# Kernel tuning notes

Hardware: AMD Instinct MI355X
Metric: run time of the kernel (lower is better)

## Reference

```python
import jax, jax.numpy as jnp
import numpy as np

SEQ = 2048
DIM = 4096
N_HEADS = 32
N_KV_HEADS = 8
HEAD_DIM = DIM // N_HEADS  # 128
ROPE_THETA = 500000.0


def setup_inputs() -> dict:
    key = jax.random.key(0)
    ks = jax.random.split(key, 5)
    s = 0.02  # keep activations numerically tame
    return {
        "x": jax.random.normal(ks[0], (SEQ, DIM), dtype=jnp.float32),
        "wq": jax.random.normal(ks[1], (DIM, DIM), dtype=jnp.float32) * s,
        "wk": jax.random.normal(ks[2], (N_KV_HEADS * HEAD_DIM, DIM), dtype=jnp.float32) * s,
        "wv": jax.random.normal(ks[3], (N_KV_HEADS * HEAD_DIM, DIM), dtype=jnp.float32) * s,
        "wo": jax.random.normal(ks[4], (DIM, DIM), dtype=jnp.float32) * s,
    }


def _rope(t):
    # t: [S, H, D]; pairs (t[...,2i], t[...,2i+1]) rotated by angle pos * theta^(-i/(D/2)),
    # matching torch.view_as_complex on x.view(S, -1, 2) * polar(1, pos*freq).
    S, H, D = t.shape
    half = D // 2
    freqs = 1.0 / (ROPE_THETA ** (jnp.arange(half, dtype=jnp.float32) / half))
    ang = jnp.arange(S, dtype=jnp.float32)[:, None] * freqs[None, :]  # [S, half]
    cos = jnp.cos(ang)[:, None, :]  # [S, 1, half]
    sin = jnp.sin(ang)[:, None, :]
    tr = t.reshape(S, H, half, 2)
    x0, x1 = tr[..., 0], tr[..., 1]
    r0 = x0 * cos - x1 * sin
    r1 = x0 * sin + x1 * cos
    return jnp.stack([r0, r1], axis=-1).reshape(S, H, D)


def reference(x, wq, wk, wv, wo):
    S = x.shape[0]
    group = N_HEADS // N_KV_HEADS
    # Per-head projections (batched over heads instead of python loop)
    q = jnp.einsum("sd,hkd->shk", x, wq.reshape(N_HEADS, HEAD_DIM, DIM))        # [S,H,D]
    k = jnp.einsum("sd,hkd->shk", x, wk.reshape(N_KV_HEADS, HEAD_DIM, DIM))     # [S,Hkv,D]
    v = jnp.einsum("sd,hkd->shk", x, wv.reshape(N_KV_HEADS, HEAD_DIM, DIM))     # [S,Hkv,D]
    q = _rope(q)
    k = _rope(k)
    # GQA: q head h uses kv head h // group -> repeat kv heads consecutively
    kf = jnp.repeat(k, group, axis=1)  # [S,H,D]
    vf = jnp.repeat(v, group, axis=1)  # [S,H,D]
    scores = jnp.einsum("shd,thd->hst", q, kf) / jnp.sqrt(jnp.float32(HEAD_DIM))
    causal = jnp.tril(jnp.ones((S, S), dtype=bool))
    scores = jnp.where(causal[None], scores, -jnp.inf)
    probs = jax.nn.softmax(scores, axis=-1)
    out = jnp.einsum("hst,thd->shd", probs, vf).reshape(S, N_HEADS * HEAD_DIM)
    return out @ wo.T
```

## Files before the change

### kernel.cpp

```cpp
#include <hip/hip_runtime.h>
#include <stdint.h>
#include <math.h>

#define SEQ   2048
#define DIM   4096
#define NHEAD 32
#define NKV   8
#define HD    128
#define KVDIM (NKV*HD)

typedef __bf16 bf16x8 __attribute__((ext_vector_type(8)));
typedef float  f32x4  __attribute__((ext_vector_type(4)));

__device__ __forceinline__ uint16_t f2bf(float f) {
  uint32_t u = __float_as_uint(f);
  uint32_t r = (u + 0x7FFFu + ((u >> 16) & 1u)) >> 16;
  return (uint16_t)r;
}
__device__ __forceinline__ bf16x8 ld_frag(const uint16_t* p) {
  return *(const bf16x8*)p;
}
__device__ __forceinline__ void async_cp16(const void* g, void* lds) {
  __builtin_amdgcn_global_load_lds(
      (const __attribute__((address_space(1))) void*)g,
      (__attribute__((address_space(3))) void*)lds, 16, 0, 0);
}

__global__ __launch_bounds__(256) void k_conv_all(
    const float* __restrict__ x, const float* __restrict__ wq,
    const float* __restrict__ wk, const float* __restrict__ wv,
    uint16_t* __restrict__ xb, uint16_t* __restrict__ wqkvb) {
  size_t i = (size_t)blockIdx.x * 256 + threadIdx.x;
  const float* s; uint16_t* d; size_t off;
  if (i < 2097152)      { s = x;  d = xb;                 off = i; }
  else if (i < 6291456) { s = wq; d = wqkvb;              off = i - 2097152; }
  else if (i < 7340032) { s = wk; d = wqkvb + 16777216u;  off = i - 6291456; }
  else                  { s = wv; d = wqkvb + 20971520u;  off = i - 7340032; }
  const float4 v = ((const float4*)s)[off];
  ushort4 o;
  o.x = f2bf(v.x); o.y = f2bf(v.y); o.z = f2bf(v.z); o.w = f2bf(v.w);
  ((ushort4*)d)[off] = o;
}

__global__ __launch_bounds__(256) void k_conv(const float* __restrict__ s,
                                              uint16_t* __restrict__ d, int n4) {
  int i = blockIdx.x * 256 + threadIdx.x;
  if (i >= n4) return;
  const float4 v = ((const float4*)s)[i];
  ushort4 o;
  o.x = f2bf(v.x); o.y = f2bf(v.y); o.z = f2bf(v.z); o.w = f2bf(v.w);
  ((ushort4*)d)[i] = o;
}

#define GEMM_PROLOGUE(A, B)                                                     \
  __shared__ __align__(16) uint16_t sA[128 * 32];                               \
  __shared__ __align__(16) uint16_t sB[128 * 32];                               \
  const int tid  = threadIdx.x;                                                 \
  const int lane = tid & 63;                                                    \
  const int wv   = tid >> 6;                                                    \
  const int quad = lane >> 4;                                                   \
  const int l16  = lane & 15;                                                   \
  const int wm   = (wv & 1) << 6;                                               \
  const int wn   = (wv >> 1) << 6;                                              \
  const int p0 = tid, p1 = tid + 256;                                           \
  const int r0 = p0 >> 2, c0 = (p0 & 3) ^ ((r0 >> 1) & 3);                      \
  const int r1 = p1 >> 2, c1 = (p1 & 3) ^ ((r1 >> 1) & 3);                      \
  const uint16_t* gA0 = A + (size_t)(m0 + r0) * DIM + c0 * 8;                   \
  const uint16_t* gA1 = A + (size_t)(m0 + r1) * DIM + c1 * 8;                   \
  const uint16_t* gB0 = B + (size_t)(n0 + r0) * DIM + c0 * 8;                   \
  const uint16_t* gB1 = B + (size_t)(n0 + r1) * DIM + c1 * 8;                   \
  uint16_t* lA0 = sA + p0 * 8;                                                  \
  uint16_t* lA1 = sA + p1 * 8;                                                  \
  uint16_t* lB0 = sB + p0 * 8;                                                  \
  uint16_t* lB1 = sB + p1 * 8;                                                  \
  f32x4 acc[4][4] = {};                                                         \
  int offA[4], offB[4];                                                         \
  _Pragma("unroll")                                                             \
  for (int t = 0; t < 4; t++) {                                                 \
    int ml_ = wm + t * 16 + l16;                                                \
    offA[t] = (ml_ * 4 + (quad ^ ((ml_ >> 1) & 3))) * 8;                        \
    int nl_ = wn + t * 16 + l16;                                                \
    offB[t] = (nl_ * 4 + (quad ^ ((nl_ >> 1) & 3))) * 8;                        \
  }                                                                             \
  for (int k0 = 0; k0 < DIM; k0 += 32) {                                        \
    async_cp16(gA0 + k0, lA0);                                                  \
    async_cp16(gA1 + k0, lA1);                                                  \
    async_cp16(gB0 + k0, lB0);                                                  \
    async_cp16(gB1 + k0, lB1);                                                  \
    __syncthreads();                                                            \
    bf16x8 af[4], bfv[4];                                                       \
    _Pragma("unroll")                                                           \
    for (int t = 0; t < 4; t++) {                                               \
      af[t]  = ld_frag(sA + offA[t]);                                           \
      bfv[t] = ld_frag(sB + offB[t]);                                           \
    }                                                                           \
    _Pragma("unroll")                                                           \
    for (int mt = 0; mt < 4; mt++)                                              \
      _Pragma("unroll")                                                         \
      for (int nt = 0; nt < 4; nt++)                                            \
        acc[mt][nt] = __builtin_amdgcn_mfma_f32_16x16x32_bf16(af[mt], bfv[nt],  \
                                                              acc[mt][nt], 0, 0, 0); \
    __syncthreads();                                                            \
  }

__global__ __launch_bounds__(256) void k_gemm_qkv(
    const uint16_t* __restrict__ xb, const uint16_t* __restrict__ wqkvb,
    uint16_t* __restrict__ Qb, uint16_t* __restrict__ Kb, uint16_t* __restrict__ Vb)
{
  const int bx = blockIdx.x;
  const int m0 = blockIdx.y * 128;
  const int n0 = bx * 128;
  GEMM_PROLOGUE(xb, wqkvb)

  const int region = (bx < 32) ? 0 : (bx < 40 ? 1 : 2);
  uint16_t* outp; int ldC, cbase;
  if (region == 0)      { outp = Qb; ldC = DIM;   cbase = n0; }
  else if (region == 1) { outp = Kb; ldC = KVDIM; cbase = n0 - 4096; }
  else                  { outp = Vb; ldC = KVDIM; cbase = n0 - 5120; }

  #pragma unroll
  for (int mt = 0; mt < 4; mt++)
    #pragma unroll
    for (int nt = 0; nt < 4; nt++) {
      const int col = cbase + wn + nt * 16 + l16;
      const int d = col & 127;
      const float freq = expf(-0.20503693f * (float)(d >> 1));
      const float sgn = (d & 1) ? 1.0f : -1.0f;
      #pragma unroll
      for (int r = 0; r < 4; r++) {
        const int row = m0 + wm + mt * 16 + quad * 4 + r;
        float v = acc[mt][nt][r];
        if (region < 2) {
          float p = __shfl_xor(v, 1, 64);
          float ang = (float)row * freq;
          float sn, cs;
          sincosf(ang, &sn, &cs);
          v = v * cs + p * sn * sgn;
        }
        outp[(size_t)row * ldC + col] = f2bf(v);
      }
    }
}

__global__ __launch_bounds__(256) void k_gemm_o(
    const uint16_t* __restrict__ ab, const uint16_t* __restrict__ wob,
    float* __restrict__ out)
{
  const int m0 = blockIdx.y * 128;
  const int n0 = blockIdx.x * 128;
  GEMM_PROLOGUE(ab, wob)
  #pragma unroll
  for (int mt = 0; mt < 4; mt++)
    #pragma unroll
    for (int nt = 0; nt < 4; nt++)
      #pragma unroll
      for (int r = 0; r < 4; r++) {
        int row = m0 + wm + mt * 16 + quad * 4 + r;
        int col = n0 + wn + nt * 16 + l16;
        out[(size_t)row * DIM + col] = acc[mt][nt][r];
      }
}

__global__ __launch_bounds__(256) void k_vtrans(const uint16_t* __restrict__ Vb,
                                                uint16_t* __restrict__ VT) {
  __shared__ uint16_t t[64][72];
  const int s0 = blockIdx.x * 64;
  const int c0 = blockIdx.y * 64;
  const int tid = threadIdx.x;
  #pragma unroll
  for (int i = 0; i < 2; i++) {
    int idx = i * 256 + tid;
    int r = idx >> 3, ch = idx & 7;
    uint4 dv = *(const uint4*)(Vb + (size_t)(s0 + r) * KVDIM + c0 + ch * 8);
    *(uint4*)(&t[r][ch * 8]) = dv;
  }
  __syncthreads();
  const int kvh = c0 >> 7;
  const int dbase = c0 & 127;
  #pragma unroll
  for (int i = 0; i < 2; i++) {
    int idx = i * 256 + tid;
    int d = idx >> 3, sc = idx & 7;
    uint16_t tmp[8];
    #pragma unroll
    for (int j2 = 0; j2 < 8; j2++) tmp[j2] = t[sc * 8 + j2][d];
    *(uint4*)(VT + (size_t)kvh * HD * SEQ + (size_t)(dbase + d) * SEQ + s0 + sc * 8) = *(const uint4*)tmp;
  }
}

#define BKV 64
#define NPAIR 40
__device__ __constant__ uint8_t c_pair[NPAIR] = {
  12,16,20,24,28,29,32,33,36,37,40,41,44,45,46,48,49,50,52,53,54,56,57,58,60,61,62,63,
  8,25,42,59,
  4,21,38,55,
  0,17,34,51
};
__device__ __constant__ uint8_t c_base[16] = {0,1,2,3,4,6,8,10,12,15,18,21,24,28,32,36};

__global__ __launch_bounds__(256) void k_flash_split(
    const uint16_t* __restrict__ Qb, const uint16_t* __restrict__ Kb,
    const uint16_t* __restrict__ VT, uint16_t* __restrict__ Opart,
    float* __restrict__ ml)
{
  const int pair = c_pair[blockIdx.x];
  const int qt   = pair >> 2;
  const int seg  = pair & 3;
  const int h    = blockIdx.y;
  const int kvh  = h >> 2;
  const int slot = h * NPAIR + c_base[qt] + seg;
  const int tid  = threadIdx.x;
  const int lane = tid & 63;
  const int wv   = tid >> 6;
  const int quad = lane >> 4;
  const int l16  = lane & 15;
  const int q0   = qt * 128;

  __shared__ __align__(16) uint16_t sK[BKV * 128];
  __shared__ __align__(16) uint16_t sVT[HD * BKV];
  __shared__ __align__(16) uint16_t sP[4 * 32 * 72];

  const uint16_t* Kbase  = Kb + kvh * HD;
  const uint16_t* VTbase = VT + (size_t)kvh * HD * SEQ;

  bf16x8 qf[2][4];
  #pragma unroll
  for (int mt = 0; mt < 2; mt++)
    #pragma unroll
    for (int ks = 0; ks < 4; ks++)
      qf[mt][ks] = ld_frag(Qb + (size_t)(q0 + wv * 32 + mt * 16 + l16) * DIM + h * HD + ks * 32 + quad * 8);

  __align__(16) uint16_t ones_bits[8];
  #pragma unroll
  for (int j = 0; j < 8; j++) ones_bits[j] = (l16 == 0) ? 0x3F80 : 0;
  const bf16x8 onesf = *(const bf16x8*)ones_bits;

  f32x4 Oacc[2][8] = {};
  f32x4 Lacc[2] = {};

  const float scale = 0.08838834764831845f;
  const float MFIX = 12.0f;
  const int j0 = seg * 8;
  const int j1 = min(j0 + 8, 2 * (qt + 1));

  for (int j = j0; j < j1; j++) {
    const int t0 = j * BKV;
    #pragma unroll
    for (int i = 0; i < 4; i++) {
      int pos = i * 256 + tid;
      int row = pos >> 4, g = (pos & 15) ^ (row & 7);
      async_cp16(Kbase + (size_t)(t0 + row) * KVDIM + g * 8, sK + pos * 8);
      int vrow = pos >> 3, vg = (pos & 7) ^ (vrow & 7);
      async_cp16(VTbase + (size_t)vrow * SEQ + t0 + vg * 8, sVT + pos * 8);
    }
    __syncthreads();

    bool active = (t0 <= q0 + wv * 32 + 31);
    if (active) {
      f32x4 Sacc[2][4] = {};
      #pragma unroll
      for (int ks = 0; ks < 4; ks++) {
        bf16x8 kf[4];
        #pragma unroll
        for (int nt = 0; nt < 4; nt++)
          kf[nt] = ld_frag(sK + (nt * 16 + l16) * 128 + (((ks * 4 + quad) ^ (l16 & 7)) * 8));
        #pragma unroll
        for (int mt = 0; mt < 2; mt++)
          #pragma unroll
          for (int nt = 0; nt < 4; nt++)
            Sacc[mt][nt] = __builtin_amdgcn_mfma_f32_16x16x32_bf16(qf[mt][ks], kf[nt], Sacc[mt][nt], 0, 0, 0);
      }
      const bool diag = (t0 + BKV - 1) > (q0 + wv * 32);
      #pragma unroll
      for (int mt = 0; mt < 2; mt++)
        #pragma unroll
        for (int nt = 0; nt < 4; nt++)
          #pragma unroll
          for (int r = 0; r < 4; r++) {
            float sv = Sacc[mt][nt][r] * scale - MFIX;
            bool msk = false;
            if (diag) {
              int qg = q0 + wv * 32 + mt * 16 + quad * 4 + r;
              int tg = t0 + nt * 16 + l16;
              msk = tg > qg;
            }
            float pv = msk ? 0.0f : __expf(sv);
            sP[(wv * 32 + mt * 16 + quad * 4 + r) * 72 + nt * 16 + l16] = f2bf(pv);
          }
      #pragma unroll
      for (int ks = 0; ks < 2; ks++) {
        bf16x8 pf[2], vf[8];
        #pragma unroll
        for (int mt = 0; mt < 2; mt++)
          pf[mt] = ld_frag(sP + (wv * 32 + mt * 16 + l16) * 72 + ks * 32 + quad * 8);
        #pragma unroll
        for (int dt = 0; dt < 8; dt++)
          vf[dt] = ld_frag(sVT + (dt * 16 + l16) * 64 + (((ks * 4 + quad) ^ (l16 & 7)) * 8));
        #pragma unroll
        for (int mt = 0; mt < 2; mt++) {
          Lacc[mt] = __builtin_amdgcn_mfma_f32_16x16x32_bf16(pf[mt], onesf, Lacc[mt], 0, 0, 0);
          #pragma unroll
          for (int dt = 0; dt < 8; dt++)
            Oacc[mt][dt] = __builtin_amdgcn_mfma_f32_16x16x32_bf16(pf[mt], vf[dt], Oacc[mt][dt], 0, 0, 0);
        }
      }
    }
    __syncthreads();
  }

  uint16_t* Op = Opart + (size_t)slot * (128 * 128);
  #pragma unroll
  for (int mt = 0; mt < 2; mt++)
    #pragma unroll
    for (int r = 0; r < 4; r++) {
      int row = wv * 32 + mt * 16 + quad * 4 + r;
      #pragma unroll
      for (int dt = 0; dt < 8; dt++)
        Op[row * 128 + dt * 16 + l16] = f2bf(Oacc[mt][dt][r]);
      if (l16 == 0)
        ml[(size_t)slot * 128 + row] = Lacc[mt][r];
    }
}

__global__ __launch_bounds__(256) void k_combine(
    const uint16_t* __restrict__ Opart, const float* __restrict__ ml,
    uint16_t* __restrict__ attnb)
{
  const int qt = blockIdx.x;
  const int h  = blockIdx.y;
  const int nseg = (qt >> 2) + 1;
  const int slot0 = h * NPAIR + c_base[qt];
  const int tid = threadIdx.x;
  const int row = tid >> 1;
  const int dh  = (tid & 1) * 64;

  float L = 0.0f;
  #pragma unroll
  for (int i = 0; i < 4; i++)
    if (i < nseg) L += ml[(size_t)(slot0 + i) * 128 + row];
  const float invL = 1.0f / L;

  uint16_t* dst = attnb + (size_t)(qt * 128 + row) * DIM + h * HD + dh;
  #pragma unroll
  for (int c = 0; c < 8; c++) {
    int d = dh + c * 8;
    float acc[8] = {};
    #pragma unroll
    for (int i = 0; i < 4; i++) {
      if (i < nseg) {
        bf16x8 v = ld_frag(Opart + (size_t)(slot0 + i) * (128 * 128) + row * 128 + d);
        #pragma unroll
        for (int j = 0; j < 8; j++) acc[j] += (float)v[j];
      }
    }
    uint16_t outv[8];
    #pragma unroll
    for (int j = 0; j < 8; j++) outv[j] = f2bf(acc[j] * invL);
    *(uint4*)(dst + c * 8) = *(const uint4*)outv;
  }
}

extern "C" void kernel_launch(void* const* d_in, const int* in_sizes, int n_in,
                              void* d_out, int out_size, void* d_ws, size_t ws_size,
                              hipStream_t stream) {
  const float* x  = (const float*)d_in[0];
  const float* wq = (const float*)d_in[1];
  const float* wk = (const float*)d_in[2];
  const float* wv = (const float*)d_in[3];
  const float* wo = (const float*)d_in[4];
  float* out = (float*)d_out;

  uint8_t* ws = (uint8_t*)d_ws;
  uint16_t* xb     = (uint16_t*)(ws + 0);
  uint16_t* wqkvb  = (uint16_t*)(ws + 16777216ull);
  uint16_t* Qb     = (uint16_t*)(ws + 67108864ull);
  uint16_t* Kb     = (uint16_t*)(ws + 83886080ull);
  uint16_t* Vb     = (uint16_t*)(ws + 88080384ull);
  uint16_t* VT     = (uint16_t*)(ws + 16777216ull);
  uint16_t* Opart  = (uint16_t*)(ws + 20971520ull);
  float*    mlbuf  = (float*)   (ws + 62914560ull);
  uint16_t* wob    = (uint16_t*)(ws + 16777216ull);
  uint16_t* attnb  = xb;

  k_conv_all<<<32768, 256, 0, stream>>>(x, wq, wk, wv, xb, wqkvb);
  k_gemm_qkv<<<dim3(48, 16), 256, 0, stream>>>(xb, wqkvb, Qb, Kb, Vb);
  k_vtrans<<<dim3(32, 16), 256, 0, stream>>>(Vb, VT);
  k_flash_split<<<dim3(NPAIR, 32), 256, 0, stream>>>(Qb, Kb, VT, Opart, mlbuf);
  k_combine<<<dim3(16, 32), 256, 0, stream>>>(Opart, mlbuf, attnb);
  k_conv<<<16384, 256, 0, stream>>>(wo, wob, 4194304);
  k_gemm_o<<<dim3(32, 16), 256, 0, stream>>>(attnb, wob, out);
}
```

Baseline: 660.1 us.

## Use 256x256 GEMM tiles with four-stage async LDS pipeline and priority scheduling

Replaces the 128x128 single-buffered GEMM mainloop used by the QKV and output projections with a 256x256 tile, 512-thread block that prefetches two k-steps ahead into a four-slot LDS ring. Loads are interleaved with MFMA work, using split barriers, waitcnt control and setprio to hide global latency and cut per-step synchronisation. The larger tiles raise data reuse per block but shrink the grid to 192 and 128 blocks and use 128 KB of LDS per block. That may leave compute units idle or limit occupancy.

```diff
diff --git a/kernel.cpp b/kernel.cpp
--- a/kernel.cpp
+++ b/kernel.cpp
@@ -52,74 +52,122 @@
   ((ushort4*)d)[i] = o;
 }
 
-#define GEMM_PROLOGUE(A, B)                                                     \
-  __shared__ __align__(16) uint16_t sA[128 * 32];                               \
-  __shared__ __align__(16) uint16_t sB[128 * 32];                               \
+#define G256_TB   8192
+
+#define G256_PROLOGUE(Aptr, Bptr)                                               \
+  __shared__ __align__(16) uint16_t sA[4 * G256_TB];                            \
+  __shared__ __align__(16) uint16_t sB[4 * G256_TB];                            \
   const int tid  = threadIdx.x;                                                 \
   const int lane = tid & 63;                                                    \
   const int wv   = tid >> 6;                                                    \
   const int quad = lane >> 4;                                                   \
   const int l16  = lane & 15;                                                   \
-  const int wm   = (wv & 1) << 6;                                               \
-  const int wn   = (wv >> 1) << 6;                                              \
-  const int p0 = tid, p1 = tid + 256;                                           \
-  const int r0 = p0 >> 2, c0 = (p0 & 3) ^ ((r0 >> 1) & 3);                      \
-  const int r1 = p1 >> 2, c1 = (p1 & 3) ^ ((r1 >> 1) & 3);                      \
-  const uint16_t* gA0 = A + (size_t)(m0 + r0) * DIM + c0 * 8;                   \
-  const uint16_t* gA1 = A + (size_t)(m0 + r1) * DIM + c1 * 8;                   \
-  const uint16_t* gB0 = B + (size_t)(n0 + r0) * DIM + c0 * 8;                   \
-  const uint16_t* gB1 = B + (size_t)(n0 + r1) * DIM + c1 * 8;                   \
-  uint16_t* lA0 = sA + p0 * 8;                                                  \
-  uint16_t* lA1 = sA + p1 * 8;                                                  \
-  uint16_t* lB0 = sB + p0 * 8;                                                  \
-  uint16_t* lB1 = sB + p1 * 8;                                                  \
-  f32x4 acc[4][4] = {};                                                         \
-  int offA[4], offB[4];                                                         \
+  const int wm   = (wv >> 2) << 7;                                \
+  const int wn   = (wv & 3) << 6;                             \
+  const uint16_t* gA = Aptr + (size_t)m0 * DIM;                                 \
+  const uint16_t* gB = Bptr + (size_t)n0 * DIM;                                 \
+  const int srow0 = tid >> 2;                                                   \
+  const int sc0   = (tid & 3) ^ ((srow0 >> 1) & 3);                             \
+  const int srow1 = (512 + tid) >> 2;                                           \
+  const int sc1   = (tid & 3) ^ ((srow1 >> 1) & 3);                             \
+  const size_t sga0 = (size_t)srow0 * DIM + sc0 * 8;                            \
+  const size_t sga1 = (size_t)srow1 * DIM + sc1 * 8;                            \
+  int offA[8], offB[4];                                                         \
+  _Pragma("unroll")                                                             \
+  for (int t = 0; t < 8; t++) {                                                 \
+    int r_ = wm + t * 16 + l16;                                                 \
+    offA[t] = r_ * 32 + (quad ^ ((r_ >> 1) & 3)) * 8;                           \
+  }                                                                             \
   _Pragma("unroll")                                                             \
   for (int t = 0; t < 4; t++) {                                                 \
-    int ml_ = wm + t * 16 + l16;                                                \
-    offA[t] = (ml_ * 4 + (quad ^ ((ml_ >> 1) & 3))) * 8;                        \
-    int nl_ = wn + t * 16 + l16;                                                \
-    offB[t] = (nl_ * 4 + (quad ^ ((nl_ >> 1) & 3))) * 8;                        \
+    int r_ = wn + t * 16 + l16;                                                 \
+    offB[t] = r_ * 32 + (quad ^ ((r_ >> 1) & 3)) * 8;                           \
   }                                                                             \
-  for (int k0 = 0; k0 < DIM; k0 += 32) {                                        \
-    async_cp16(gA0 + k0, lA0);                                                  \
-    async_cp16(gA1 + k0, lA1);                                                  \
-    async_cp16(gB0 + k0, lB0);                                                  \
-    async_cp16(gB1 + k0, lB1);                                                  \
-    __syncthreads();                                                            \
-    bf16x8 af[4], bfv[4];                                                       \
+  f32x4 acc[8][4] = {};                                                         \
+                                             \
+  async_cp16(gA + sga0,      sA + tid * 8);                                     \
+  async_cp16(gB + sga0,      sB + tid * 8);                                     \
+  async_cp16(gA + sga1,      sA + 4096 + tid * 8);                              \
+  async_cp16(gB + sga1,      sB + 4096 + tid * 8);                              \
+  async_cp16(gA + sga0 + 32, sA + G256_TB + tid * 8);                           \
+  async_cp16(gB + sga0 + 32, sB + G256_TB + tid * 8);                           \
+  async_cp16(gA + sga1 + 32, sA + G256_TB + 4096 + tid * 8);                    \
+  async_cp16(gB + sga1 + 32, sB + G256_TB + 4096 + tid * 8);                    \
+  asm volatile("s_waitcnt vmcnt(4)" ::: "memory");            \
+  __builtin_amdgcn_s_barrier();                                                 \
+  for (int T = 0; T < 128; T++) {                                               \
+    const int cb = (T & 3) * G256_TB;                                           \
+    const uint16_t* bA = sA + cb;                                               \
+    const uint16_t* bB = sB + cb;                                               \
+    const int  k2 = (T + 2) * 32;                                               \
+    const bool pf = (T + 2 < 128);                                              \
+    const int  db = ((T + 2) & 3) * G256_TB;                                    \
+              \
+    bf16x8 af0[4], bfv[4];                                                      \
     _Pragma("unroll")                                                           \
     for (int t = 0; t < 4; t++) {                                               \
-      af[t]  = ld_frag(sA + offA[t]);                                           \
-      bfv[t] = ld_frag(sB + offB[t]);                                           \
+      af0[t] = ld_frag(bA + offA[t]);                                           \
+      bfv[t] = ld_frag(bB + offB[t]);                                           \
     }                                                                           \
+    if (pf) {                                                                   \
+      async_cp16(gA + sga0 + k2, sA + db + tid * 8);                            \
+      async_cp16(gB + sga0 + k2, sB + db + tid * 8);                            \
+    }                                                                           \
+    __builtin_amdgcn_s_barrier();                                               \
+    asm volatile("s_waitcnt lgkmcnt(0)" ::: "memory");                          \
+    __builtin_amdgcn_sched_barrier(0);                                          \
+    __builtin_amdgcn_s_setprio(1);                                              \
     _Pragma("unroll")                                                           \
     for (int mt = 0; mt < 4; mt++)                                              \
       _Pragma("unroll")                                                         \
       for (int nt = 0; nt < 4; nt++)                                            \
-        acc[mt][nt] = __builtin_amdgcn_mfma_f32_16x16x32_bf16(af[mt], bfv[nt],  \
+        acc[mt][nt] = __builtin_amdgcn_mfma_f32_16x16x32_bf16(af0[mt], bfv[nt], \
                                                               acc[mt][nt], 0, 0, 0); \
-    __syncthreads();                                                            \
+    __builtin_amdgcn_s_setprio(0);                                              \
+    __builtin_amdgcn_s_barrier();                                               \
+              \
+    bf16x8 af1[4];                                                              \
+    _Pragma("unroll")                                                           \
+    for (int t = 0; t < 4; t++)                                                 \
+      af1[t] = ld_frag(bA + offA[4 + t]);                                       \
+    if (pf) {                                                                   \
+      async_cp16(gA + sga1 + k2, sA + db + 4096 + tid * 8);                     \
+      async_cp16(gB + sga1 + k2, sB + db + 4096 + tid * 8);                     \
+    }                                                                           \
+    __builtin_amdgcn_s_barrier();                                               \
+    asm volatile("s_waitcnt lgkmcnt(0)" ::: "memory");                          \
+    __builtin_amdgcn_sched_barrier(0);                                          \
+    __builtin_amdgcn_s_setprio(1);                                              \
+    _Pragma("unroll")                                                           \
+    for (int mt = 0; mt < 4; mt++)                                              \
+      _Pragma("unroll")                                                         \
+      for (int nt = 0; nt < 4; nt++)                                            \
+        acc[4 + mt][nt] = __builtin_amdgcn_mfma_f32_16x16x32_bf16(af1[mt], bfv[nt], \
+                                                                  acc[4 + mt][nt], 0, 0, 0); \
+    __builtin_amdgcn_s_setprio(0);                                              \
+          \
+    if (pf) { asm volatile("s_waitcnt vmcnt(4)" ::: "memory"); }                \
+    else    { asm volatile("s_waitcnt vmcnt(0)" ::: "memory"); }                \
+    __builtin_amdgcn_s_barrier();                                               \
   }
 
-__global__ __launch_bounds__(256) void k_gemm_qkv(
+__global__ __launch_bounds__(512, 2) void k_gemm_qkv(
     const uint16_t* __restrict__ xb, const uint16_t* __restrict__ wqkvb,
     uint16_t* __restrict__ Qb, uint16_t* __restrict__ Kb, uint16_t* __restrict__ Vb)
 {
   const int bx = blockIdx.x;
-  const int m0 = blockIdx.y * 128;
-  const int n0 = bx * 128;
-  GEMM_PROLOGUE(xb, wqkvb)
-
-  const int region = (bx < 32) ? 0 : (bx < 40 ? 1 : 2);
+  const int m0 = blockIdx.y * 256;
+  const int n0 = bx * 256;
+  G256_PROLOGUE(xb, wqkvb)
+
+  const int region = (bx < 16) ? 0 : (bx < 20 ? 1 : 2);
   uint16_t* outp; int ldC, cbase;
   if (region == 0)      { outp = Qb; ldC = DIM;   cbase = n0; }
   else if (region == 1) { outp = Kb; ldC = KVDIM; cbase = n0 - 4096; }
   else                  { outp = Vb; ldC = KVDIM; cbase = n0 - 5120; }
 
   #pragma unroll
-  for (int mt = 0; mt < 4; mt++)
+  for (int mt = 0; mt < 8; mt++)
     #pragma unroll
     for (int nt = 0; nt < 4; nt++) {
       const int col = cbase + wn + nt * 16 + l16;
@@ -142,15 +190,15 @@
     }
 }
 
-__global__ __launch_bounds__(256) void k_gemm_o(
+__global__ __launch_bounds__(512, 2) void k_gemm_o(
     const uint16_t* __restrict__ ab, const uint16_t* __restrict__ wob,
     float* __restrict__ out)
 {
-  const int m0 = blockIdx.y * 128;
-  const int n0 = blockIdx.x * 128;
-  GEMM_PROLOGUE(ab, wob)
-  #pragma unroll
-  for (int mt = 0; mt < 4; mt++)
+  const int m0 = blockIdx.y * 256;
+  const int n0 = blockIdx.x * 256;
+  G256_PROLOGUE(ab, wob)
+  #pragma unroll
+  for (int mt = 0; mt < 8; mt++)
     #pragma unroll
     for (int nt = 0; nt < 4; nt++)
       #pragma unroll
@@ -383,10 +431,10 @@
   uint16_t* attnb  = xb;
 
   k_conv_all<<<32768, 256, 0, stream>>>(x, wq, wk, wv, xb, wqkvb);
-  k_gemm_qkv<<<dim3(48, 16), 256, 0, stream>>>(xb, wqkvb, Qb, Kb, Vb);
+  k_gemm_qkv<<<dim3(24, 8), 512, 0, stream>>>(xb, wqkvb, Qb, Kb, Vb);
   k_vtrans<<<dim3(32, 16), 256, 0, stream>>>(Vb, VT);
   k_flash_split<<<dim3(NPAIR, 32), 256, 0, stream>>>(Qb, Kb, VT, Opart, mlbuf);
   k_combine<<<dim3(16, 32), 256, 0, stream>>>(Opart, mlbuf, attnb);
   k_conv<<<16384, 256, 0, stream>>>(wo, wob, 4194304);
-  k_gemm_o<<<dim3(32, 16), 256, 0, stream>>>(attnb, wob, out);
-}
+  k_gemm_o<<<dim3(16, 8), 512, 0, stream>>>(attnb, wob, out);
+}
```

New measurement: 626.5 us. -5.1%, faster.
